# Performance work log

Measured on AMD Instinct MI355X. Metric: run time of the kernel, lower is better.

The kernel has to match this reference:

```python
import jax, jax.numpy as jnp
import numpy as np


def _top2_margin(logits, targets):
    # logits: [N, C], targets: [N] int
    top2, _ = jax.lax.top_k(logits, 2)                       # [N, 2]
    tgt_logit = jnp.take_along_axis(logits, targets[:, None], axis=1)[:, 0]  # [N]
    # margin = top1 - top2 if the target class attains the max, else 0
    return jnp.where(tgt_logit == top2[:, 0], top2[:, 0] - top2[:, 1],
                     jnp.zeros((), dtype=logits.dtype))


def setup_inputs() -> dict:
    key = jax.random.key(0)
    ks = jax.random.split(key, 6)
    N, C = 16384, 1000
    return {
        "outputs1": jax.random.normal(ks[0], (N, C), dtype=jnp.float32),
        "outputs2": jax.random.normal(ks[1], (N, C), dtype=jnp.float32),
        "outputs3": jax.random.normal(ks[2], (N, C), dtype=jnp.float32),
        "outputs4": jax.random.normal(ks[3], (N, C), dtype=jnp.float32),
        "mimic": jax.random.normal(ks[4], (N, C), dtype=jnp.float32),
        "targets": jax.random.randint(ks[5], (N,), 0, C, dtype=jnp.int64),
        "n_test": N,
    }


def reference(outputs1, outputs2, outputs3, outputs4, mimic, targets, n_test):
    T = 2.0  # temperature (init kwarg)
    # n_test == N; the loop over samples is fully vectorized here.
    margins = jnp.stack([
        _top2_margin(outputs1, targets),
        _top2_margin(outputs2, targets),
        _top2_margin(outputs3, targets),
        _top2_margin(outputs4, targets),
        _top2_margin(mimic, targets),
    ], axis=1)                                               # [N, 5]
    out_threshold = jax.nn.softmax(margins / T, axis=1)      # [N, 5]
    max_preds = jnp.maximum(jnp.maximum(outputs1.max(), outputs2.max()),
                            jnp.maximum(outputs3.max(), outputs4.max()))
    return (max_preds, out_threshold)
```

## Files before the change

### kernel.cpp

```cpp
#include <hip/hip_runtime.h>
#include <math.h>

#define NROWS 16384
#define NCOLS 1000
#define NQ    250
#define NMAT  5
#define PAIRS (NROWS * NMAT)
#define WPB   4
#define BLOCKS_A (PAIRS / WPB)

__global__ __launch_bounds__(256) void margins_kernel(
    const float* __restrict__ o0, const float* __restrict__ o1,
    const float* __restrict__ o2, const float* __restrict__ o3,
    const float* __restrict__ o4, const int* __restrict__ targets,
    float* __restrict__ margins, float* __restrict__ blockmax)
{
    const int wave = threadIdx.x >> 6;
    const int lane = threadIdx.x & 63;
    const int p    = blockIdx.x * WPB + wave;
    const int m    = p >> 14;
    const int row  = p & (NROWS - 1);

    const float* mat = (m == 0) ? o0 : (m == 1) ? o1 : (m == 2) ? o2
                       : (m == 3) ? o3 : o4;
    const float*  rowp = mat + (size_t)row * NCOLS;
    const float4* base = (const float4*)rowp;

    float4 v0 = base[lane];
    float4 v1 = base[lane + 64];
    float4 v2 = base[lane + 128];
    float4 v3 = make_float4(-INFINITY, -INFINITY, -INFINITY, -INFINITY);
    if (lane < (NQ - 192)) v3 = base[lane + 192];

    float t1 = -INFINITY, t2 = -INFINITY;
#define UPD(x) { float _mn = fminf(t1, (x)); t1 = fmaxf(t1, (x)); t2 = fmaxf(t2, _mn); }
    UPD(v0.x) UPD(v0.y) UPD(v0.z) UPD(v0.w)
    UPD(v1.x) UPD(v1.y) UPD(v1.z) UPD(v1.w)
    UPD(v2.x) UPD(v2.y) UPD(v2.z) UPD(v2.w)
    UPD(v3.x) UPD(v3.y) UPD(v3.z) UPD(v3.w)
#undef UPD

    #pragma unroll
    for (int off = 32; off > 0; off >>= 1) {
        float a1 = __shfl_xor(t1, off);
        float a2 = __shfl_xor(t2, off);
        float mn = fminf(t1, a1);
        t1 = fmaxf(t1, a1);
        t2 = fmaxf(fmaxf(t2, a2), mn);
    }

    if (lane == 0) {
        const int   t   = targets[row];
        const float tgt = rowp[t];
        const float margin = (tgt == t1) ? (t1 - t2) : 0.0f;
        margins[row * NMAT + m] = margin;
    }

    __shared__ float smax[WPB];
    if (lane == 0) smax[wave] = (m < 4) ? t1 : -INFINITY;
    __syncthreads();
    if (threadIdx.x == 0) {
        blockmax[blockIdx.x] =
            fmaxf(fmaxf(smax[0], smax[1]), fmaxf(smax[2], smax[3]));
    }
}

__global__ __launch_bounds__(256) void softmax_kernel(
    const float* __restrict__ margins, const float* __restrict__ blockmax,
    float* __restrict__ out)
{
    const int row = blockIdx.x * 256 + threadIdx.x;

    float mg[NMAT];
    #pragma unroll
    for (int j = 0; j < NMAT; ++j) mg[j] = margins[row * NMAT + j];

    float mx = mg[0];
    #pragma unroll
    for (int j = 1; j < NMAT; ++j) mx = fmaxf(mx, mg[j]);

    float e[NMAT];
    float s = 0.0f;
    #pragma unroll
    for (int j = 0; j < NMAT; ++j) { e[j] = expf((mg[j] - mx) * 0.5f); s += e[j]; }
    const float inv = 1.0f / s;
    #pragma unroll
    for (int j = 0; j < NMAT; ++j) out[1 + row * NMAT + j] = e[j] * inv;

    if (blockIdx.x == 0) {
        __shared__ float red[256];
        float mm = -INFINITY;
        for (int k = threadIdx.x; k < BLOCKS_A; k += 256)
            mm = fmaxf(mm, blockmax[k]);
        red[threadIdx.x] = mm;
        __syncthreads();
        #pragma unroll
        for (int s2 = 128; s2 > 0; s2 >>= 1) {
            if (threadIdx.x < s2)
                red[threadIdx.x] = fmaxf(red[threadIdx.x], red[threadIdx.x + s2]);
            __syncthreads();
        }
        if (threadIdx.x == 0) out[0] = red[0];
    }
}

extern "C" void kernel_launch(void* const* d_in, const int* in_sizes, int n_in,
                              void* d_out, int out_size, void* d_ws, size_t ws_size,
                              hipStream_t stream) {
    const float* o0 = (const float*)d_in[0];
    const float* o1 = (const float*)d_in[1];
    const float* o2 = (const float*)d_in[2];
    const float* o3 = (const float*)d_in[3];
    const float* o4 = (const float*)d_in[4];
    const int*   tg = (const int*)d_in[5];
    float* out = (float*)d_out;

    float* margins  = (float*)d_ws;
    float* blockmax = margins + PAIRS;

    margins_kernel<<<BLOCKS_A, 256, 0, stream>>>(o0, o1, o2, o3, o4, tg,
                                                 margins, blockmax);
    softmax_kernel<<<64, 256, 0, stream>>>(margins, blockmax, out);
}
```

Baseline: 301.6 us.

## Fuse five-matrix margin computation with softmax, one wave per row

Each wave now handles one row across all five matrices and loads all 20 float4s up front. It then computes the softmax in lane 0, so the intermediate margins buffer and its global round trip go away. The separate softmax kernel shrinks to a single-block max reduction. This raises memory-level parallelism per wave and removes intermediate traffic, but it uses more registers, which may lower occupancy. It also cuts the number of blocks fivefold.

```diff
diff --git a/kernel.cpp b/kernel.cpp
--- a/kernel.cpp
+++ b/kernel.cpp
@@ -3,105 +3,116 @@
 
 #define NROWS 16384
 #define NCOLS 1000
-#define NQ    250
 #define NMAT  5
-#define PAIRS (NROWS * NMAT)
 #define WPB   4
-#define BLOCKS_A (PAIRS / WPB)
+#define BLOCKS_A (NROWS / WPB)
 
-__global__ __launch_bounds__(256) void margins_kernel(
+__global__ __launch_bounds__(256) void fused_kernel(
     const float* __restrict__ o0, const float* __restrict__ o1,
     const float* __restrict__ o2, const float* __restrict__ o3,
     const float* __restrict__ o4, const int* __restrict__ targets,
-    float* __restrict__ margins, float* __restrict__ blockmax)
+    float* __restrict__ out, float* __restrict__ blockmax)
 {
     const int wave = threadIdx.x >> 6;
     const int lane = threadIdx.x & 63;
-    const int p    = blockIdx.x * WPB + wave;
-    const int m    = p >> 14;
-    const int row  = p & (NROWS - 1);
+    const int row  = blockIdx.x * WPB + wave;
 
-    const float* mat = (m == 0) ? o0 : (m == 1) ? o1 : (m == 2) ? o2
-                       : (m == 3) ? o3 : o4;
-    const float*  rowp = mat + (size_t)row * NCOLS;
-    const float4* base = (const float4*)rowp;
+    const float* rows[NMAT];
+    rows[0] = o0 + (size_t)row * NCOLS;
+    rows[1] = o1 + (size_t)row * NCOLS;
+    rows[2] = o2 + (size_t)row * NCOLS;
+    rows[3] = o3 + (size_t)row * NCOLS;
+    rows[4] = o4 + (size_t)row * NCOLS;
 
-    float4 v0 = base[lane];
-    float4 v1 = base[lane + 64];
-    float4 v2 = base[lane + 128];
-    float4 v3 = make_float4(-INFINITY, -INFINITY, -INFINITY, -INFINITY);
-    if (lane < (NQ - 192)) v3 = base[lane + 192];
+    float4 v[NMAT][4];
+    #pragma unroll
+    for (int m = 0; m < NMAT; ++m) {
+        const float4* b = (const float4*)rows[m];
+        v[m][0] = b[lane];
+        v[m][1] = b[lane + 64];
+        v[m][2] = b[lane + 128];
+        v[m][3] = make_float4(-INFINITY, -INFINITY, -INFINITY, -INFINITY);
+    }
+    if (lane < 58) {
+        #pragma unroll
+        for (int m = 0; m < NMAT; ++m)
+            v[m][3] = ((const float4*)rows[m])[lane + 192];
+    }
 
-    float t1 = -INFINITY, t2 = -INFINITY;
-#define UPD(x) { float _mn = fminf(t1, (x)); t1 = fmaxf(t1, (x)); t2 = fmaxf(t2, _mn); }
-    UPD(v0.x) UPD(v0.y) UPD(v0.z) UPD(v0.w)
-    UPD(v1.x) UPD(v1.y) UPD(v1.z) UPD(v1.w)
-    UPD(v2.x) UPD(v2.y) UPD(v2.z) UPD(v2.w)
-    UPD(v3.x) UPD(v3.y) UPD(v3.z) UPD(v3.w)
+    float t1[NMAT], t2[NMAT];
+#define UPD(m, x) { float _mn = fminf(t1[m], (x)); t1[m] = fmaxf(t1[m], (x)); \
+                    t2[m] = fmaxf(t2[m], _mn); }
+    #pragma unroll
+    for (int m = 0; m < NMAT; ++m) {
+        t1[m] = -INFINITY; t2[m] = -INFINITY;
+        #pragma unroll
+        for (int q = 0; q < 4; ++q) {
+            UPD(m, v[m][q].x) UPD(m, v[m][q].y)
+            UPD(m, v[m][q].z) UPD(m, v[m][q].w)
+        }
+    }
 #undef UPD
 
     #pragma unroll
     for (int off = 32; off > 0; off >>= 1) {
-        float a1 = __shfl_xor(t1, off);
-        float a2 = __shfl_xor(t2, off);
-        float mn = fminf(t1, a1);
-        t1 = fmaxf(t1, a1);
-        t2 = fmaxf(fmaxf(t2, a2), mn);
+        float a1[NMAT], a2[NMAT];
+        #pragma unroll
+        for (int m = 0; m < NMAT; ++m) {
+            a1[m] = __shfl_xor(t1[m], off);
+            a2[m] = __shfl_xor(t2[m], off);
+        }
+        #pragma unroll
+        for (int m = 0; m < NMAT; ++m) {
+            float mn = fminf(t1[m], a1[m]);
+            t1[m] = fmaxf(t1[m], a1[m]);
+            t2[m] = fmaxf(fmaxf(t2[m], a2[m]), mn);
+        }
     }
 
     if (lane == 0) {
-        const int   t   = targets[row];
-        const float tgt = rowp[t];
-        const float margin = (tgt == t1) ? (t1 - t2) : 0.0f;
-        margins[row * NMAT + m] = margin;
+        const int t = targets[row];
+        float mg[NMAT];
+        #pragma unroll
+        for (int m = 0; m < NMAT; ++m) {
+            const float tgt = rows[m][t];
+            mg[m] = (tgt == t1[m]) ? (t1[m] - t2[m]) : 0.0f;
+        }
+        float mx = mg[0];
+        #pragma unroll
+        for (int m = 1; m < NMAT; ++m) mx = fmaxf(mx, mg[m]);
+        float e[NMAT], s = 0.0f;
+        #pragma unroll
+        for (int m = 0; m < NMAT; ++m) { e[m] = __expf((mg[m] - mx) * 0.5f); s += e[m]; }
+        const float inv = 1.0f / s;
+        #pragma unroll
+        for (int m = 0; m < NMAT; ++m) out[1 + row * NMAT + m] = e[m] * inv;
     }
 
     __shared__ float smax[WPB];
-    if (lane == 0) smax[wave] = (m < 4) ? t1 : -INFINITY;
+    if (lane == 0)
+        smax[wave] = fmaxf(fmaxf(t1[0], t1[1]), fmaxf(t1[2], t1[3]));
     __syncthreads();
-    if (threadIdx.x == 0) {
+    if (threadIdx.x == 0)
         blockmax[blockIdx.x] =
             fmaxf(fmaxf(smax[0], smax[1]), fmaxf(smax[2], smax[3]));
-    }
 }
 
-__global__ __launch_bounds__(256) void softmax_kernel(
-    const float* __restrict__ margins, const float* __restrict__ blockmax,
-    float* __restrict__ out)
+__global__ __launch_bounds__(256) void reduce_kernel(
+    const float* __restrict__ blockmax, float* __restrict__ out)
 {
-    const int row = blockIdx.x * 256 + threadIdx.x;
-
-    float mg[NMAT];
+    __shared__ float red[256];
+    float mm = -INFINITY;
+    for (int k = threadIdx.x; k < BLOCKS_A; k += 256)
+        mm = fmaxf(mm, blockmax[k]);
+    red[threadIdx.x] = mm;
+    __syncthreads();
     #pragma unroll
-    for (int j = 0; j < NMAT; ++j) mg[j] = margins[row * NMAT + j];
-
-    float mx = mg[0];
-    #pragma unroll
-    for (int j = 1; j < NMAT; ++j) mx = fmaxf(mx, mg[j]);
-
-    float e[NMAT];
-    float s = 0.0f;
-    #pragma unroll
-    for (int j = 0; j < NMAT; ++j) { e[j] = expf((mg[j] - mx) * 0.5f); s += e[j]; }
-    const float inv = 1.0f / s;
-    #pragma unroll
-    for (int j = 0; j < NMAT; ++j) out[1 + row * NMAT + j] = e[j] * inv;
-
-    if (blockIdx.x == 0) {
-        __shared__ float red[256];
-        float mm = -INFINITY;
-        for (int k = threadIdx.x; k < BLOCKS_A; k += 256)
-            mm = fmaxf(mm, blockmax[k]);
-        red[threadIdx.x] = mm;
+    for (int s = 128; s > 0; s >>= 1) {
+        if (threadIdx.x < s)
+            red[threadIdx.x] = fmaxf(red[threadIdx.x], red[threadIdx.x + s]);
         __syncthreads();
-        #pragma unroll
-        for (int s2 = 128; s2 > 0; s2 >>= 1) {
-            if (threadIdx.x < s2)
-                red[threadIdx.x] = fmaxf(red[threadIdx.x], red[threadIdx.x + s2]);
-            __syncthreads();
-        }
-        if (threadIdx.x == 0) out[0] = red[0];
     }
+    if (threadIdx.x == 0) out[0] = red[0];
 }
 
 extern "C" void kernel_launch(void* const* d_in, const int* in_sizes, int n_in,
@@ -115,10 +126,9 @@
     const int*   tg = (const int*)d_in[5];
     float* out = (float*)d_out;
 
-    float* margins  = (float*)d_ws;
-    float* blockmax = margins + PAIRS;
+    float* blockmax = (float*)d_ws;
 
-    margins_kernel<<<BLOCKS_A, 256, 0, stream>>>(o0, o1, o2, o3, o4, tg,
-                                                 margins, blockmax);
-    softmax_kernel<<<64, 256, 0, stream>>>(margins, blockmax, out);
+    fused_kernel<<<BLOCKS_A, 256, 0, stream>>>(o0, o1, o2, o3, o4, tg,
+                                               out, blockmax);
+    reduce_kernel<<<1, 256, 0, stream>>>(blockmax, out);
 }
```

Result: faster. 293.6 us (-2.7%).
